# Performance work log

Hardware: AMD Instinct MI355X
Metric: run time of the kernel (lower is better)

## Reference

```python
import math
import jax, jax.numpy as jnp
import numpy as np

B, L, DIM, H = 2, 2048, 1024, 16
D = DIM // H  # head_dim = 64
EPS = 1e-6


def setup_inputs() -> dict:
    key = jax.random.key(0)
    ks = jax.random.split(key, 5)
    s = 0.02
    return {
        "x": jax.random.normal(ks[0], (B, L, DIM), jnp.float32),
        "pe": jax.random.normal(ks[1], (B, 1, L, D // 2, 2, 2), jnp.float32),
        "w_qkv": jax.random.normal(ks[2], (DIM, 3 * DIM), jnp.float32) * s,
        "q_scale": jnp.ones((D,), jnp.float32),
        "k_scale": jnp.ones((D,), jnp.float32),
        "w_proj": jax.random.normal(ks[3], (DIM, DIM), jnp.float32) * s,
        "b_proj": jnp.zeros((DIM,), jnp.float32),
    }


def _rmsnorm(t, scale):
    # flax nnx.RMSNorm: x * rsqrt(mean(x^2) + eps) * scale, over last dim
    var = jnp.mean(jnp.square(t), axis=-1, keepdims=True)
    return t * jax.lax.rsqrt(var + EPS) * scale


def _apply_rope(t, pe):
    # t: [B,H,L,D]; pe: [B,1,L,D/2,2,2]
    t2 = t.reshape(*t.shape[:-1], D // 2, 1, 2)
    out = pe[..., 0] * t2[..., 0] + pe[..., 1] * t2[..., 1]  # [B,H,L,D/2,2]
    return out.reshape(t.shape)


def reference(x, pe, w_qkv, q_scale, k_scale, w_proj, b_proj):
    # fused QKV projection
    qkv = jnp.einsum('bld,de->ble', x, w_qkv)  # [B,L,3*DIM]
    qkv = qkv.reshape(B, L, 3, H, D).transpose(2, 0, 3, 1, 4)  # [3,B,H,L,D]
    q, k, v = qkv[0], qkv[1], qkv[2]
    # QK RMSNorm
    q = _rmsnorm(q, q_scale)
    k = _rmsnorm(k, k_scale)
    # RoPE via pe
    q = _apply_rope(q, pe)
    k = _apply_rope(k, pe)
    # scaled dot product attention
    scores = jnp.einsum('bhqd,bhkd->bhqk', q, k) / math.sqrt(D)
    attn = jax.nn.softmax(scores, axis=-1)
    o = jnp.einsum('bhqk,bhkd->bhqd', attn, v)  # [B,H,L,D]
    o = o.transpose(0, 2, 1, 3).reshape(B, L, DIM)  # B H L D -> B L (H D)
    # output projection
    return jnp.einsum('bld,de->ble', o, w_proj) + b_proj
```

## Files before the change

kernel.cpp:

```cpp
#include <hip/hip_runtime.h>
#include <math.h>

#define BB 2
#define LL 2048
#define DIMM 1024
#define HH 16
#define DD 64
#define QKV_N 3072

typedef unsigned short u16;
typedef unsigned int u32;
typedef __attribute__((ext_vector_type(8))) short short8;
typedef __attribute__((ext_vector_type(4))) float f32x4;

__device__ __forceinline__ float bf2f(u16 h) {
    unsigned u = ((unsigned)h) << 16;
    return __uint_as_float(u);
}
__device__ __forceinline__ u16 f2bf(float f) {
    unsigned u = __float_as_uint(f);
    u += 0x7fffu + ((u >> 16) & 1u);
    return (u16)(u >> 16);
}
__device__ __forceinline__ u32 pack_bf2(float lo, float hi) {
    u32 a = __float_as_uint(hi) + 0x8000u;
    u32 b = __float_as_uint(lo) + 0x8000u;
    return __builtin_amdgcn_perm(a, b, 0x07060302u);
}

__global__ __launch_bounds__(256) void convx(
    const float* __restrict__ X, u16* __restrict__ Xb)
{
    int i = (blockIdx.x * 256 + threadIdx.x) * 8;
    float4 a = *(const float4*)&X[i];
    float4 b = *(const float4*)&X[i + 4];
    u16 t[8] = {f2bf(a.x), f2bf(a.y), f2bf(a.z), f2bf(a.w),
                f2bf(b.x), f2bf(b.y), f2bf(b.z), f2bf(b.w)};
    *(uint4*)&Xb[i] = *(uint4*)t;
}

__global__ __launch_bounds__(256) void convt(
    const float* __restrict__ W, u16* __restrict__ Wt, int K, int N)
{
    __shared__ u16 s[64][72];
    const int tid = threadIdx.x;
    const int k0 = blockIdx.x * 64, n0 = blockIdx.y * 64;
#pragma unroll
    for (int t = 0; t < 16; ++t) {
        int flat = t * 256 + tid;
        int kk = flat >> 6, nn = flat & 63;
        s[nn][kk] = f2bf(W[(size_t)(k0 + kk) * N + n0 + nn]);
    }
    __syncthreads();
#pragma unroll
    for (int t = 0; t < 2; ++t) {
        int chunk = t * 256 + tid;
        int nn = chunk >> 3, kc = chunk & 7;
        *(uint4*)&Wt[(size_t)(n0 + nn) * K + k0 + kc * 8] = *(uint4*)&s[nn][kc * 8];
    }
}

__global__ __launch_bounds__(256) void vtrans(
    const u16* __restrict__ qkv, u16* __restrict__ vt)
{
    __shared__ u16 s[64][72];
    const int tid = threadIdx.x;
    const int bh = blockIdx.y;
    const int b = bh >> 4, h = bh & 15;
    const int l0 = blockIdx.x * 64;
    const u16* vbase = qkv + (size_t)b * LL * QKV_N + 2048 + h * 64;
#pragma unroll
    for (int t = 0; t < 2; ++t) {
        int flat = t * 2048 + tid * 8;
        int l = flat >> 6, d = flat & 63;
        *(uint4*)&s[l][d] = *(const uint4*)&vbase[(size_t)(l0 + l) * QKV_N + d];
    }
    __syncthreads();
#pragma unroll
    for (int t = 0; t < 2; ++t) {
        int flat = t * 2048 + tid * 8;
        int d = flat >> 6, l = flat & 63;
        u16 tmp[8];
#pragma unroll
        for (int j = 0; j < 8; ++j) tmp[j] = s[l + j][d];
        *(uint4*)&vt[((size_t)bh * 64 + d) * LL + l0 + l] = *(uint4*)tmp;
    }
}

template <bool BIAS, bool OUTBF>
__global__ __launch_bounds__(256) void gemm_mfma(
    const u16* __restrict__ A, const u16* __restrict__ Bt,
    const float* __restrict__ bias, void* __restrict__ Cv,
    int M, int N, int K)
{
    __shared__ u16 sA[128 * 72];
    __shared__ u16 sB[128 * 72];

    const int tid = threadIdx.x;
    const int wave = tid >> 6, lane = tid & 63;
    const int mIdx = lane & 15, quad = lane >> 4;
    const int wr = wave >> 1, wc = wave & 1;
    const int m0 = blockIdx.y * 128, n0 = blockIdx.x * 128;

    f32x4 acc[4][4];
#pragma unroll
    for (int a = 0; a < 4; ++a)
#pragma unroll
        for (int b = 0; b < 4; ++b) acc[a][b] = (f32x4){0.f, 0.f, 0.f, 0.f};

    for (int k0 = 0; k0 < K; k0 += 64) {
#pragma unroll
        for (int t = 0; t < 4; ++t) {
            int ci = t * 256 + tid;
            int row = ci >> 3, kc = ci & 7;
            *(uint4*)&sA[row * 72 + kc * 8] =
                *(const uint4*)&A[(size_t)(m0 + row) * K + k0 + kc * 8];
            *(uint4*)&sB[row * 72 + kc * 8] =
                *(const uint4*)&Bt[(size_t)(n0 + row) * K + k0 + kc * 8];
        }
        __syncthreads();
#pragma unroll
        for (int ks = 0; ks < 2; ++ks) {
            short8 af[4], bfr[4];
#pragma unroll
            for (int mt = 0; mt < 4; ++mt)
                af[mt] = *(const short8*)&sA[(64 * wr + 16 * mt + mIdx) * 72 + ks * 32 + quad * 8];
#pragma unroll
            for (int nt = 0; nt < 4; ++nt)
                bfr[nt] = *(const short8*)&sB[(64 * wc + 16 * nt + mIdx) * 72 + ks * 32 + quad * 8];
#pragma unroll
            for (int mt = 0; mt < 4; ++mt)
#pragma unroll
                for (int nt = 0; nt < 4; ++nt)
                    acc[mt][nt] = __builtin_amdgcn_mfma_f32_16x16x32_bf16(
                        af[mt], bfr[nt], acc[mt][nt], 0, 0, 0);
        }
        __syncthreads();
    }

#pragma unroll
    for (int mt = 0; mt < 4; ++mt) {
#pragma unroll
        for (int r = 0; r < 4; ++r) {
            int row = m0 + 64 * wr + 16 * mt + quad * 4 + r;
#pragma unroll
            for (int nt = 0; nt < 4; ++nt) {
                int col = n0 + 64 * wc + 16 * nt + mIdx;
                float v = acc[mt][nt][r];
                if (BIAS) v += bias[col];
                if (OUTBF) ((u16*)Cv)[(size_t)row * N + col] = f2bf(v);
                else       ((float*)Cv)[(size_t)row * N + col] = v;
            }
        }
    }
}

__global__ __launch_bounds__(256) void rmsrope(
    u16* __restrict__ qkv, const float* __restrict__ pe,
    const float* __restrict__ qs, const float* __restrict__ ks)
{
    const int gtid = blockIdx.x * 256 + threadIdx.x;
    const int w = gtid >> 6;
    const int lane = gtid & 63;
    const int h = w & 15;
    const int bl = w >> 4;

    u16* base = qkv + (size_t)bl * QKV_N + h * 64 + lane;
    float qv = bf2f(base[0]);
    float kv = bf2f(base[1024]);

    float sq = qv * qv, sk = kv * kv;
#pragma unroll
    for (int off = 32; off >= 1; off >>= 1) {
        sq += __shfl_xor(sq, off);
        sk += __shfl_xor(sk, off);
    }
    qv = qv * rsqrtf(sq * (1.f / 64.f) + 1e-6f) * qs[lane];
    kv = kv * rsqrtf(sk * (1.f / 64.f) + 1e-6f) * ks[lane];

    const float* peb = pe + ((size_t)bl * 32 + (lane >> 1)) * 4 + (lane & 1) * 2;
    float p0 = peb[0], p1 = peb[1];

    float qp = __shfl_xor(qv, 1);
    float kp = __shfl_xor(kv, 1);
    bool odd = (lane & 1);
    float qe = odd ? qp : qv, qo = odd ? qv : qp;
    float ke = odd ? kp : kv, ko = odd ? kv : kp;

    base[0]    = f2bf((p0 * qe + p1 * qo) * 0.18033688011112042f);
    base[1024] = f2bf(p0 * ke + p1 * ko);
}

#define PR 72

__global__ __launch_bounds__(512, 4) void attn_mfma(
    const u16* __restrict__ qkv, const u16* __restrict__ vt, u16* __restrict__ o)
{
    __shared__ u16 sK[2][64 * PR];
    __shared__ u16 sVt[2][64 * PR];
    __shared__ u16 sP[128 * PR];

    const int tid = threadIdx.x;
    const int wave = tid >> 6;
    const int lane = tid & 63;
    const int mIdx = lane & 15;
    const int quad = lane >> 4;

    const int bh = blockIdx.x >> 4;
    const int qt = blockIdx.x & 15;
    const int b = bh >> 4, h = bh & 15;
    const int q0 = qt * 128;

    const u16* kbase = qkv + (size_t)b * LL * QKV_N + 1024 + h * 64;
    const u16* vbase = vt + (size_t)bh * 64 * LL;

    const u16* qrow = qkv + (size_t)b * LL * QKV_N + h * 64
                      + (size_t)(q0 + 16 * wave + mIdx) * QKV_N;
    short8 aq0 = *(const short8*)&qrow[quad * 8];
    short8 aq1 = *(const short8*)&qrow[32 + quad * 8];

    const int sr = tid >> 3;
    const int sc = (tid & 7) * 8;

    {
        uint4 kv4 = *(const uint4*)&kbase[(size_t)sr * QKV_N + sc];
        uint4 vv4 = *(const uint4*)&vbase[(size_t)sr * LL + sc];
        *(uint4*)&sK[0][sr * PR + sc] = kv4;
        *(uint4*)&sVt[0][sr * PR + sc] = vv4;
    }

    float lsum = 0.f;
    f32x4 Oacc[4];
#pragma unroll
    for (int nb = 0; nb < 4; ++nb) Oacc[nb] = (f32x4){0.f, 0.f, 0.f, 0.f};

    u16* sProw = &sP[(16 * wave + mIdx) * PR];

    for (int kt = 0; kt < 32; ++kt) {
        const int p = kt & 1;
        __syncthreads();

        if (kt + 1 < 32) {
            const int k0n = (kt + 1) * 64;
            uint4 kv4 = *(const uint4*)&kbase[(size_t)(k0n + sr) * QKV_N + sc];
            uint4 vv4 = *(const uint4*)&vbase[(size_t)sr * LL + k0n + sc];
            *(uint4*)&sK[p ^ 1][sr * PR + sc] = kv4;
            *(uint4*)&sVt[p ^ 1][sr * PR + sc] = vv4;
        }

#pragma unroll
        for (int nb = 0; nb < 4; ++nb) {
            short8 bk0 = *(const short8*)&sK[p][(16 * nb + mIdx) * PR + quad * 8];
            short8 bk1 = *(const short8*)&sK[p][(16 * nb + mIdx) * PR + 32 + quad * 8];
            f32x4 st = (f32x4){0.f, 0.f, 0.f, 0.f};
            st = __builtin_amdgcn_mfma_f32_16x16x32_bf16(bk0, aq0, st, 0, 0, 0);
            st = __builtin_amdgcn_mfma_f32_16x16x32_bf16(bk1, aq1, st, 0, 0, 0);

            float p0 = exp2f(st[0]), p1 = exp2f(st[1]);
            float p2 = exp2f(st[2]), p3 = exp2f(st[3]);
            lsum += (p0 + p1) + (p2 + p3);
            u32 w0 = pack_bf2(p0, p1);
            u32 w1 = pack_bf2(p2, p3);
            uint2 wpair; wpair.x = w0; wpair.y = w1;
            *(uint2*)&sProw[16 * nb + quad * 4] = wpair;
        }

        short8 pa0 = *(const short8*)&sProw[quad * 8];
        short8 pa1 = *(const short8*)&sProw[32 + quad * 8];
#pragma unroll
        for (int nb = 0; nb < 4; ++nb) {
            short8 bv0 = *(const short8*)&sVt[p][(16 * nb + mIdx) * PR + quad * 8];
            short8 bv1 = *(const short8*)&sVt[p][(16 * nb + mIdx) * PR + 32 + quad * 8];
            Oacc[nb] = __builtin_amdgcn_mfma_f32_16x16x32_bf16(pa0, bv0, Oacc[nb], 0, 0, 0);
            Oacc[nb] = __builtin_amdgcn_mfma_f32_16x16x32_bf16(pa1, bv1, Oacc[nb], 0, 0, 0);
        }
    }

    lsum += __shfl_xor(lsum, 16);
    lsum += __shfl_xor(lsum, 32);

#pragma unroll
    for (int r = 0; r < 4; ++r) {
        float lr = __shfl(lsum, quad * 4 + r);
        float linv = 1.f / lr;
        int rowg = b * LL + q0 + 16 * wave + quad * 4 + r;
#pragma unroll
        for (int nb = 0; nb < 4; ++nb) {
            o[(size_t)rowg * DIMM + h * 64 + 16 * nb + mIdx] = f2bf(Oacc[nb][r] * linv);
        }
    }
}

extern "C" void kernel_launch(void* const* d_in, const int* in_sizes, int n_in,
                              void* d_out, int out_size, void* d_ws, size_t ws_size,
                              hipStream_t stream) {
    const float* x       = (const float*)d_in[0];
    const float* pe      = (const float*)d_in[1];
    const float* w_qkv   = (const float*)d_in[2];
    const float* q_scale = (const float*)d_in[3];
    const float* k_scale = (const float*)d_in[4];
    const float* w_proj  = (const float*)d_in[5];
    const float* b_proj  = (const float*)d_in[6];
    float* out = (float*)d_out;

    char* ws = (char*)d_ws;
    u16* qkv    = (u16*)ws;  ws += (size_t)4096 * 3072 * 2;
    u16* o      = (u16*)ws;  ws += (size_t)4096 * 1024 * 2;
    u16* xb     = (u16*)ws;  ws += (size_t)4096 * 1024 * 2;
    u16* wqkvt  = (u16*)ws;  ws += (size_t)3072 * 1024 * 2;
    u16* wprojt = (u16*)ws;  ws += (size_t)1024 * 1024 * 2;
    u16* vtbuf  = (u16*)ws;  ws += (size_t)BB * HH * DD * LL * 2;

    convx<<<(4096 * 1024) / (256 * 8), 256, 0, stream>>>(x, xb);
    convt<<<dim3(1024 / 64, QKV_N / 64), 256, 0, stream>>>(w_qkv, wqkvt, DIMM, QKV_N);
    convt<<<dim3(1024 / 64, 1024 / 64), 256, 0, stream>>>(w_proj, wprojt, DIMM, DIMM);

    gemm_mfma<false, true><<<dim3(QKV_N / 128, (BB * LL) / 128), 256, 0, stream>>>(
        xb, wqkvt, nullptr, qkv, BB * LL, QKV_N, DIMM);

    rmsrope<<<(BB * LL * HH) / 4, 256, 0, stream>>>(qkv, pe, q_scale, k_scale);

    vtrans<<<dim3(LL / 64, BB * HH), 256, 0, stream>>>(qkv, vtbuf);

    attn_mfma<<<BB * HH * (LL / 128), 512, 0, stream>>>(qkv, vtbuf, o);

    gemm_mfma<true, false><<<dim3(DIMM / 128, (BB * LL) / 128), 256, 0, stream>>>(
        o, wprojt, b_proj, out, BB * LL, DIMM, DIMM);
}
```

Measured before the change: 237.8 us.

## Fuse RMSNorm+RoPE into QKV GEMM epilogue and rewrite attention with 32x32 MFMA

Removes the separate rmsrope kernel by doing per-head RMS normalization and RoPE inside the QKV GEMM epilogue, using shuffles across the 16-lane column groups. The attention kernel is rewritten to use 32x32x16 MFMA with 256-query tiles and register-prefetched, single-buffered K/V in shared memory. Output is staged through LDS for coalesced 16-byte stores. The GEMM is split into two specialized kernels. Risks include the extra sync per tile from single buffering and lower block count (256 blocks) for attention.

```diff
diff --git a/kernel.cpp b/kernel.cpp
--- a/kernel.cpp
+++ b/kernel.cpp
@@ -12,6 +12,7 @@
 typedef unsigned int u32;
 typedef __attribute__((ext_vector_type(8))) short short8;
 typedef __attribute__((ext_vector_type(4))) float f32x4;
+typedef __attribute__((ext_vector_type(16))) float f32x16;
 
 __device__ __forceinline__ float bf2f(u16 h) {
     unsigned u = ((unsigned)h) << 16;
@@ -26,6 +27,12 @@
     u32 a = __float_as_uint(hi) + 0x8000u;
     u32 b = __float_as_uint(lo) + 0x8000u;
     return __builtin_amdgcn_perm(a, b, 0x07060302u);
+}
+__device__ __forceinline__ f32x16 zero16() {
+    f32x16 z;
+#pragma unroll
+    for (int i = 0; i < 16; ++i) z[i] = 0.f;
+    return z;
 }
 
 __global__ __launch_bounds__(256) void convx(
@@ -87,11 +94,10 @@
     }
 }
 
-template <bool BIAS, bool OUTBF>
-__global__ __launch_bounds__(256) void gemm_mfma(
+__global__ __launch_bounds__(256) void gemm_qkv(
     const u16* __restrict__ A, const u16* __restrict__ Bt,
-    const float* __restrict__ bias, void* __restrict__ Cv,
-    int M, int N, int K)
+    u16* __restrict__ C, const float* __restrict__ pe,
+    const float* __restrict__ qs, const float* __restrict__ ks)
 {
     __shared__ u16 sA[128 * 72];
     __shared__ u16 sB[128 * 72];
@@ -101,6 +107,7 @@
     const int mIdx = lane & 15, quad = lane >> 4;
     const int wr = wave >> 1, wc = wave & 1;
     const int m0 = blockIdx.y * 128, n0 = blockIdx.x * 128;
+    const int N = QKV_N, K = DIMM;
 
     f32x4 acc[4][4];
 #pragma unroll
@@ -120,14 +127,14 @@
         }
         __syncthreads();
 #pragma unroll
-        for (int ks = 0; ks < 2; ++ks) {
+        for (int ks2 = 0; ks2 < 2; ++ks2) {
             short8 af[4], bfr[4];
 #pragma unroll
             for (int mt = 0; mt < 4; ++mt)
-                af[mt] = *(const short8*)&sA[(64 * wr + 16 * mt + mIdx) * 72 + ks * 32 + quad * 8];
+                af[mt] = *(const short8*)&sA[(64 * wr + 16 * mt + mIdx) * 72 + ks2 * 32 + quad * 8];
 #pragma unroll
             for (int nt = 0; nt < 4; ++nt)
-                bfr[nt] = *(const short8*)&sB[(64 * wc + 16 * nt + mIdx) * 72 + ks * 32 + quad * 8];
+                bfr[nt] = *(const short8*)&sB[(64 * wc + 16 * nt + mIdx) * 72 + ks2 * 32 + quad * 8];
 #pragma unroll
             for (int mt = 0; mt < 4; ++mt)
 #pragma unroll
@@ -138,155 +145,230 @@
         __syncthreads();
     }
 
-#pragma unroll
-    for (int mt = 0; mt < 4; ++mt) {
+    if (n0 >= 2048) {
+#pragma unroll
+        for (int mt = 0; mt < 4; ++mt)
+#pragma unroll
+            for (int r = 0; r < 4; ++r) {
+                int row = m0 + 64 * wr + 16 * mt + quad * 4 + r;
+#pragma unroll
+                for (int nt = 0; nt < 4; ++nt) {
+                    int col = n0 + 64 * wc + 16 * nt + mIdx;
+                    C[(size_t)row * N + col] = f2bf(acc[mt][nt][r]);
+                }
+            }
+    } else {
+        const float* scv = (n0 < 1024) ? qs : ks;
+        const float pre = (n0 < 1024) ? 0.18033688011112042f : 1.0f;
+        float scl[4];
+#pragma unroll
+        for (int nt = 0; nt < 4; ++nt) scl[nt] = scv[16 * nt + mIdx];
+
+#pragma unroll
+        for (int mt = 0; mt < 4; ++mt) {
+#pragma unroll
+            for (int r = 0; r < 4; ++r) {
+                float s = 0.f;
+#pragma unroll
+                for (int nt = 0; nt < 4; ++nt) {
+                    float a = acc[mt][nt][r];
+                    s += a * a;
+                }
+                s += __shfl_xor(s, 1);
+                s += __shfl_xor(s, 2);
+                s += __shfl_xor(s, 4);
+                s += __shfl_xor(s, 8);
+                float rn = rsqrtf(s * (1.f / 64.f) + 1e-6f);
+                int R = m0 + 64 * wr + 16 * mt + quad * 4 + r;
+                size_t peo = (size_t)R * 128;
+#pragma unroll
+                for (int nt = 0; nt < 4; ++nt) {
+                    float v = acc[mt][nt][r] * rn * scl[nt];
+                    float pp = __shfl_xor(v, 1);
+                    float2 pw = *(const float2*)&pe[peo + 2 * (16 * nt + mIdx)];
+                    float e  = (mIdx & 1) ? pp : v;
+                    float od = (mIdx & 1) ? v : pp;
+                    C[(size_t)R * N + n0 + 64 * wc + 16 * nt + mIdx] =
+                        f2bf((pw.x * e + pw.y * od) * pre);
+                }
+            }
+        }
+    }
+}
+
+__global__ __launch_bounds__(256) void gemm_proj(
+    const u16* __restrict__ A, const u16* __restrict__ Bt,
+    const float* __restrict__ bias, float* __restrict__ C)
+{
+    __shared__ u16 sA[128 * 72];
+    __shared__ u16 sB[128 * 72];
+
+    const int tid = threadIdx.x;
+    const int wave = tid >> 6, lane = tid & 63;
+    const int mIdx = lane & 15, quad = lane >> 4;
+    const int wr = wave >> 1, wc = wave & 1;
+    const int m0 = blockIdx.y * 128, n0 = blockIdx.x * 128;
+    const int N = DIMM, K = DIMM;
+
+    f32x4 acc[4][4];
+#pragma unroll
+    for (int a = 0; a < 4; ++a)
+#pragma unroll
+        for (int b = 0; b < 4; ++b) acc[a][b] = (f32x4){0.f, 0.f, 0.f, 0.f};
+
+    for (int k0 = 0; k0 < K; k0 += 64) {
+#pragma unroll
+        for (int t = 0; t < 4; ++t) {
+            int ci = t * 256 + tid;
+            int row = ci >> 3, kc = ci & 7;
+            *(uint4*)&sA[row * 72 + kc * 8] =
+                *(const uint4*)&A[(size_t)(m0 + row) * K + k0 + kc * 8];
+            *(uint4*)&sB[row * 72 + kc * 8] =
+                *(const uint4*)&Bt[(size_t)(n0 + row) * K + k0 + kc * 8];
+        }
+        __syncthreads();
+#pragma unroll
+        for (int ks2 = 0; ks2 < 2; ++ks2) {
+            short8 af[4], bfr[4];
+#pragma unroll
+            for (int mt = 0; mt < 4; ++mt)
+                af[mt] = *(const short8*)&sA[(64 * wr + 16 * mt + mIdx) * 72 + ks2 * 32 + quad * 8];
+#pragma unroll
+            for (int nt = 0; nt < 4; ++nt)
+                bfr[nt] = *(const short8*)&sB[(64 * wc + 16 * nt + mIdx) * 72 + ks2 * 32 + quad * 8];
+#pragma unroll
+            for (int mt = 0; mt < 4; ++mt)
+#pragma unroll
+                for (int nt = 0; nt < 4; ++nt)
+                    acc[mt][nt] = __builtin_amdgcn_mfma_f32_16x16x32_bf16(
+                        af[mt], bfr[nt], acc[mt][nt], 0, 0, 0);
+        }
+        __syncthreads();
+    }
+
+#pragma unroll
+    for (int mt = 0; mt < 4; ++mt)
 #pragma unroll
         for (int r = 0; r < 4; ++r) {
             int row = m0 + 64 * wr + 16 * mt + quad * 4 + r;
 #pragma unroll
             for (int nt = 0; nt < 4; ++nt) {
                 int col = n0 + 64 * wc + 16 * nt + mIdx;
-                float v = acc[mt][nt][r];
-                if (BIAS) v += bias[col];
-                if (OUTBF) ((u16*)Cv)[(size_t)row * N + col] = f2bf(v);
-                else       ((float*)Cv)[(size_t)row * N + col] = v;
-            }
-        }
-    }
-}
-
-__global__ __launch_bounds__(256) void rmsrope(
-    u16* __restrict__ qkv, const float* __restrict__ pe,
-    const float* __restrict__ qs, const float* __restrict__ ks)
-{
-    const int gtid = blockIdx.x * 256 + threadIdx.x;
-    const int w = gtid >> 6;
-    const int lane = gtid & 63;
-    const int h = w & 15;
-    const int bl = w >> 4;
-
-    u16* base = qkv + (size_t)bl * QKV_N + h * 64 + lane;
-    float qv = bf2f(base[0]);
-    float kv = bf2f(base[1024]);
-
-    float sq = qv * qv, sk = kv * kv;
-#pragma unroll
-    for (int off = 32; off >= 1; off >>= 1) {
-        sq += __shfl_xor(sq, off);
-        sk += __shfl_xor(sk, off);
-    }
-    qv = qv * rsqrtf(sq * (1.f / 64.f) + 1e-6f) * qs[lane];
-    kv = kv * rsqrtf(sk * (1.f / 64.f) + 1e-6f) * ks[lane];
-
-    const float* peb = pe + ((size_t)bl * 32 + (lane >> 1)) * 4 + (lane & 1) * 2;
-    float p0 = peb[0], p1 = peb[1];
-
-    float qp = __shfl_xor(qv, 1);
-    float kp = __shfl_xor(kv, 1);
-    bool odd = (lane & 1);
-    float qe = odd ? qp : qv, qo = odd ? qv : qp;
-    float ke = odd ? kp : kv, ko = odd ? kv : kp;
-
-    base[0]    = f2bf((p0 * qe + p1 * qo) * 0.18033688011112042f);
-    base[1024] = f2bf(p0 * ke + p1 * ko);
-}
-
-#define PR 72
-
-__global__ __launch_bounds__(512, 4) void attn_mfma(
+                C[(size_t)row * N + col] = acc[mt][nt][r] + bias[col];
+            }
+        }
+}
+
+#define KPR 70
+#define PPR 66
+
+__global__ __launch_bounds__(512) void attn_mfma32(
     const u16* __restrict__ qkv, const u16* __restrict__ vt, u16* __restrict__ o)
 {
-    __shared__ u16 sK[2][64 * PR];
-    __shared__ u16 sVt[2][64 * PR];
-    __shared__ u16 sP[128 * PR];
+    __shared__ u16 sK[64 * KPR];
+    __shared__ u16 sVt[64 * KPR];
+    __shared__ u16 sP[256 * PPR];
 
     const int tid = threadIdx.x;
     const int wave = tid >> 6;
     const int lane = tid & 63;
-    const int mIdx = lane & 15;
-    const int quad = lane >> 4;
-
-    const int bh = blockIdx.x >> 4;
-    const int qt = blockIdx.x & 15;
+    const int m32 = lane & 31;
+    const int half = lane >> 5;
+
+    const int bh = blockIdx.x >> 3;
+    const int qt = blockIdx.x & 7;
     const int b = bh >> 4, h = bh & 15;
-    const int q0 = qt * 128;
+    const int q0 = qt * 256;
 
     const u16* kbase = qkv + (size_t)b * LL * QKV_N + 1024 + h * 64;
     const u16* vbase = vt + (size_t)bh * 64 * LL;
 
-    const u16* qrow = qkv + (size_t)b * LL * QKV_N + h * 64
-                      + (size_t)(q0 + 16 * wave + mIdx) * QKV_N;
-    short8 aq0 = *(const short8*)&qrow[quad * 8];
-    short8 aq1 = *(const short8*)&qrow[32 + quad * 8];
-
-    const int sr = tid >> 3;
-    const int sc = (tid & 7) * 8;
+    const u16* qrow = qkv + ((size_t)(b * LL + q0 + 32 * wave + m32)) * QKV_N + h * 64;
+    short8 qf[4];
+#pragma unroll
+    for (int s = 0; s < 4; ++s) qf[s] = *(const short8*)&qrow[16 * s + 8 * half];
+
+    const int sr = tid >> 3, sc = (tid & 7) * 8;
+
+    uint4 kreg = *(const uint4*)&kbase[(size_t)sr * QKV_N + sc];
+    uint4 vreg = *(const uint4*)&vbase[(size_t)sr * LL + sc];
+
+    float lsum = 0.f;
+    f32x16 Oacc[2] = {zero16(), zero16()};
+
+    u16* sProw = &sP[(32 * wave + m32) * PPR];
+
+    for (int kt = 0; kt < 32; ++kt) {
+        *(uint4*)&sK[sr * KPR + sc] = kreg;
+        *(uint4*)&sVt[sr * KPR + sc] = vreg;
+        __syncthreads();
+
+        if (kt + 1 < 32) {
+            kreg = *(const uint4*)&kbase[(size_t)((kt + 1) * 64 + sr) * QKV_N + sc];
+            vreg = *(const uint4*)&vbase[(size_t)sr * LL + (kt + 1) * 64 + sc];
+        }
+
+        f32x16 st[2] = {zero16(), zero16()};
+#pragma unroll
+        for (int s = 0; s < 4; ++s) {
+#pragma unroll
+            for (int mt = 0; mt < 2; ++mt) {
+                short8 kf = *(const short8*)&sK[(32 * mt + m32) * KPR + 16 * s + 8 * half];
+                st[mt] = __builtin_amdgcn_mfma_f32_32x32x16_bf16(kf, qf[s], st[mt], 0, 0, 0);
+            }
+        }
+
+#pragma unroll
+        for (int mt = 0; mt < 2; ++mt) {
+            float p[16];
+#pragma unroll
+            for (int i = 0; i < 16; ++i) {
+                p[i] = exp2f(st[mt][i]);
+                lsum += p[i];
+            }
+#pragma unroll
+            for (int g = 0; g < 4; ++g) {
+                uint2 pr;
+                pr.x = pack_bf2(p[4 * g + 0], p[4 * g + 1]);
+                pr.y = pack_bf2(p[4 * g + 2], p[4 * g + 3]);
+                *(uint2*)&sProw[32 * mt + 4 * half + 8 * g] = pr;
+            }
+        }
+
+#pragma unroll
+        for (int s = 0; s < 4; ++s) {
+            short8 pf = *(const short8*)&sProw[16 * s + 8 * half];
+#pragma unroll
+            for (int dt = 0; dt < 2; ++dt) {
+                short8 vf = *(const short8*)&sVt[(32 * dt + m32) * KPR + 16 * s + 8 * half];
+                Oacc[dt] = __builtin_amdgcn_mfma_f32_32x32x16_bf16(vf, pf, Oacc[dt], 0, 0, 0);
+            }
+        }
+        __syncthreads();
+    }
+
+    lsum += __shfl_xor(lsum, 32);
+    float linv = 1.f / lsum;
+
+#pragma unroll
+    for (int dt = 0; dt < 2; ++dt) {
+#pragma unroll
+        for (int g = 0; g < 4; ++g) {
+            uint2 pr;
+            pr.x = pack_bf2(Oacc[dt][4 * g + 0] * linv, Oacc[dt][4 * g + 1] * linv);
+            pr.y = pack_bf2(Oacc[dt][4 * g + 2] * linv, Oacc[dt][4 * g + 3] * linv);
+            *(uint2*)&sProw[32 * dt + 4 * half + 8 * g] = pr;
+        }
+    }
+    __syncthreads();
 
     {
-        uint4 kv4 = *(const uint4*)&kbase[(size_t)sr * QKV_N + sc];
-        uint4 vv4 = *(const uint4*)&vbase[(size_t)sr * LL + sc];
-        *(uint4*)&sK[0][sr * PR + sc] = kv4;
-        *(uint4*)&sVt[0][sr * PR + sc] = vv4;
-    }
-
-    float lsum = 0.f;
-    f32x4 Oacc[4];
-#pragma unroll
-    for (int nb = 0; nb < 4; ++nb) Oacc[nb] = (f32x4){0.f, 0.f, 0.f, 0.f};
-
-    u16* sProw = &sP[(16 * wave + mIdx) * PR];
-
-    for (int kt = 0; kt < 32; ++kt) {
-        const int p = kt & 1;
-        __syncthreads();
-
-        if (kt + 1 < 32) {
-            const int k0n = (kt + 1) * 64;
-            uint4 kv4 = *(const uint4*)&kbase[(size_t)(k0n + sr) * QKV_N + sc];
-            uint4 vv4 = *(const uint4*)&vbase[(size_t)sr * LL + k0n + sc];
-            *(uint4*)&sK[p ^ 1][sr * PR + sc] = kv4;
-            *(uint4*)&sVt[p ^ 1][sr * PR + sc] = vv4;
-        }
-
-#pragma unroll
-        for (int nb = 0; nb < 4; ++nb) {
-            short8 bk0 = *(const short8*)&sK[p][(16 * nb + mIdx) * PR + quad * 8];
-            short8 bk1 = *(const short8*)&sK[p][(16 * nb + mIdx) * PR + 32 + quad * 8];
-            f32x4 st = (f32x4){0.f, 0.f, 0.f, 0.f};
-            st = __builtin_amdgcn_mfma_f32_16x16x32_bf16(bk0, aq0, st, 0, 0, 0);
-            st = __builtin_amdgcn_mfma_f32_16x16x32_bf16(bk1, aq1, st, 0, 0, 0);
-
-            float p0 = exp2f(st[0]), p1 = exp2f(st[1]);
-            float p2 = exp2f(st[2]), p3 = exp2f(st[3]);
-            lsum += (p0 + p1) + (p2 + p3);
-            u32 w0 = pack_bf2(p0, p1);
-            u32 w1 = pack_bf2(p2, p3);
-            uint2 wpair; wpair.x = w0; wpair.y = w1;
-            *(uint2*)&sProw[16 * nb + quad * 4] = wpair;
-        }
-
-        short8 pa0 = *(const short8*)&sProw[quad * 8];
-        short8 pa1 = *(const short8*)&sProw[32 + quad * 8];
-#pragma unroll
-        for (int nb = 0; nb < 4; ++nb) {
-            short8 bv0 = *(const short8*)&sVt[p][(16 * nb + mIdx) * PR + quad * 8];
-            short8 bv1 = *(const short8*)&sVt[p][(16 * nb + mIdx) * PR + 32 + quad * 8];
-            Oacc[nb] = __builtin_amdgcn_mfma_f32_16x16x32_bf16(pa0, bv0, Oacc[nb], 0, 0, 0);
-            Oacc[nb] = __builtin_amdgcn_mfma_f32_16x16x32_bf16(pa1, bv1, Oacc[nb], 0, 0, 0);
-        }
-    }
-
-    lsum += __shfl_xor(lsum, 16);
-    lsum += __shfl_xor(lsum, 32);
-
-#pragma unroll
-    for (int r = 0; r < 4; ++r) {
-        float lr = __shfl(lsum, quad * 4 + r);
-        float linv = 1.f / lr;
-        int rowg = b * LL + q0 + 16 * wave + quad * 4 + r;
-#pragma unroll
-        for (int nb = 0; nb < 4; ++nb) {
-            o[(size_t)rowg * DIMM + h * 64 + 16 * nb + mIdx] = f2bf(Oacc[nb][r] * linv);
+        const int row = tid >> 1, seg = tid & 1;
+        size_t gbase = (size_t)(b * LL + q0 + row) * DIMM + h * 64 + 32 * seg;
+#pragma unroll
+        for (int c = 0; c < 4; ++c) {
+            uint4 v = *(const uint4*)&sP[row * PPR + 32 * seg + 8 * c];
+            *(uint4*)&o[gbase + 8 * c] = v;
         }
     }
 }
@@ -315,15 +397,13 @@
     convt<<<dim3(1024 / 64, QKV_N / 64), 256, 0, stream>>>(w_qkv, wqkvt, DIMM, QKV_N);
     convt<<<dim3(1024 / 64, 1024 / 64), 256, 0, stream>>>(w_proj, wprojt, DIMM, DIMM);
 
-    gemm_mfma<false, true><<<dim3(QKV_N / 128, (BB * LL) / 128), 256, 0, stream>>>(
-        xb, wqkvt, nullptr, qkv, BB * LL, QKV_N, DIMM);
-
-    rmsrope<<<(BB * LL * HH) / 4, 256, 0, stream>>>(qkv, pe, q_scale, k_scale);
+    gemm_qkv<<<dim3(QKV_N / 128, (BB * LL) / 128), 256, 0, stream>>>(
+        xb, wqkvt, qkv, pe, q_scale, k_scale);
 
     vtrans<<<dim3(LL / 64, BB * HH), 256, 0, stream>>>(qkv, vtbuf);
 
-    attn_mfma<<<BB * HH * (LL / 128), 512, 0, stream>>>(qkv, vtbuf, o);
-
-    gemm_mfma<true, false><<<dim3(DIMM / 128, (BB * LL) / 128), 256, 0, stream>>>(
-        o, wprojt, b_proj, out, BB * LL, DIMM, DIMM);
-}
+    attn_mfma32<<<BB * HH * (LL / 256), 512, 0, stream>>>(qkv, vtbuf, o);
+
+    gemm_proj<<<dim3(DIMM / 128, (BB * LL) / 128), 256, 0, stream>>>(
+        o, wprojt, b_proj, out);
+}
```

New measurement: 304.0 us. 27.9% more time.
